# Kernel optimization log

Hardware: AMD Instinct MI355X
Metric: run time of the kernel (lower is better)

Reference implementation:

```python
import jax, jax.numpy as jnp
import numpy as np

N, H_DIM, LATENT, MLP_H, F_OUT = 256, 128, 128, 256, 16
SUPP = 0.5  # ancestor_suppression_strength
EPS = 1e-12


def setup_inputs() -> dict:
    key = jax.random.key(0)
    ks = jax.random.split(key, 12)
    def w(k, shape):
        fan_in = shape[0]
        return jax.random.normal(k, shape, jnp.float32) / np.sqrt(fan_in)
    return {
        'z': jax.random.normal(ks[0], (LATENT,), jnp.float32),
        'targets': jax.random.randint(ks[1], (N, N), 0, 2, jnp.int32),
        'pos_emb': jax.random.normal(ks[2], (N, H_DIM), jnp.float32),
        'Ws1': w(ks[3], (H_DIM, H_DIM)),
        'Wn1': w(ks[4], (H_DIM, H_DIM)),
        'b1': jnp.zeros((H_DIM,), jnp.float32),
        'Ws2': w(ks[5], (H_DIM, H_DIM)),
        'Wn2': w(ks[6], (H_DIM, H_DIM)),
        'b2': jnp.zeros((H_DIM,), jnp.float32),
        'Wm1': w(ks[7], (LATENT + 3 * H_DIM, MLP_H)),
        'bm1': jnp.zeros((MLP_H,), jnp.float32),
        'Wm2': w(ks[8], (MLP_H, 1)),
        'bm2': jnp.zeros((1,), jnp.float32),
        'Wf': w(ks[9], (H_DIM, F_OUT)),
        'bf': jnp.zeros((F_OUT,), jnp.float32),
    }


def reference(z, targets, pos_emb, Ws1, Wn1, b1, Ws2, Wn2, b2,
              Wm1, bm1, Wm2, bm2, Wf, bf):
    tgt = jnp.tril(targets.astype(jnp.float32), -1)  # [N,N] strict lower: row=child, col=parent
    idx = jnp.arange(N)
    h0 = z  # decoder_init=None => hidden state init is z itself
    layers = ((Ws1, Wn1, b1), (Ws2, Wn2, b2))

    def gnn(Hs, M, active):
        # M[dst, src]: messages aggregated over incoming (parent) edges
        for Ws, Wn, b in layers:
            Hs = jax.nn.relu(Hs @ Ws + (M @ Hs) @ Wn + b) * active[:, None]
        return Hs

    def step(carry, t):
        Hs, anc, lp = carry
        Hs = Hs.at[t].set(h0 + pos_emb[t])          # new node t
        active = (idx <= t).astype(jnp.float32)
        M = tgt * (idx < t)[:, None].astype(jnp.float32)  # edges added in steps < t
        Hs = gnn(Hs, M, active)
        h_t = Hs[t]
        cand = (idx < t).astype(jnp.float32)        # candidate parents i < t
        mlp_in = jnp.concatenate([
            jnp.broadcast_to(h_t, (N, H_DIM)), Hs,
            jnp.broadcast_to(z, (N, LATENT)),
            jnp.broadcast_to(pos_emb[t], (N, H_DIM))], axis=1)
        logits = (jax.nn.relu(mlp_in @ Wm1 + bm1) @ Wm2 + bm2)[:, 0]
        probs = jax.nn.sigmoid(logits)
        # suppression[i] = prod_{j<t} (1 - s * anc[j][i])
        supp = jnp.prod(jnp.where((idx < t)[:, None], 1.0 - SUPP * anc, 1.0), axis=0)
        adj = probs * supp
        gt = tgt[t]
        logp = gt * jnp.log(adj + EPS) + (1.0 - gt) * jnp.log(1.0 - adj + EPS)
        lp = lp + jnp.sum(logp * cand)
        # ancestors of t = union over parents p of (anc[p] | {p})
        anc_t = jnp.minimum(1.0, gt @ anc + gt)
        anc = anc.at[t].set(anc_t)
        return (Hs, anc, lp), None

    H0 = jnp.zeros((N, H_DIM), jnp.float32).at[0].set(h0)
    anc0 = jnp.zeros((N, N), jnp.float32)
    (Hs, anc, lp), _ = jax.lax.scan(step, (H0, anc0, jnp.float32(0.0)), jnp.arange(1, N))
    # node_feature_decoder path: one more GNN pass over the full graph
    Hs = gnn(Hs, tgt, jnp.ones((N,), jnp.float32))
    X_out = Hs @ Wf + bf
    return tgt, X_out, lp
```

## Files before the change

kernel.cpp:

```cpp
#include <hip/hip_runtime.h>

#define NN 256
#define HD 128
#define GNN_NB 128
#define MLP_NB 64
#define NBLK 192
#define NTHR 512
#define D_HS 3
#define D_H1 2

#define HS_OFF 0
#define H1R_OFF 98304
#define PROG_OFF 163840
#define MF_OFF   (163840 + 4096)

#define STH_L 0
#define STM_L 256
#define PT_L  512
#define TGT_L 0
#define PTM_L 2048
#define PT3_L 10240
#define HC_L  11264
#define CT_L  11776
#define CZ_L  12032
#define W2_L  12288
#define HP_L  12544
#define PART_L 12800
#define ANC_L 13312
#define LP_L  13344
#define LDS_FLOATS 13360

__device__ __forceinline__ float2 ldc_f2(const float* p) {
    unsigned long long u = __hip_atomic_load((const unsigned long long*)p,
                                             __ATOMIC_RELAXED, __HIP_MEMORY_SCOPE_AGENT);
    float2 r;
    r.x = __uint_as_float((unsigned)u);
    r.y = __uint_as_float((unsigned)(u >> 32));
    return r;
}
__device__ __forceinline__ void stc_f(float* p, float v) {
    __hip_atomic_store((unsigned*)p, __float_as_uint(v),
                       __ATOMIC_RELAXED, __HIP_MEMORY_SCOPE_AGENT);
}
__device__ __forceinline__ unsigned ldf(const unsigned* p) {
    return __hip_atomic_load(p, __ATOMIC_RELAXED, __HIP_MEMORY_SCOPE_AGENT);
}
__device__ __forceinline__ void stf(unsigned* p, unsigned v) {
    __hip_atomic_store(p, v, __ATOMIC_RELAXED, __HIP_MEMORY_SCOPE_AGENT);
}

__device__ __forceinline__ void bar_lds() {
    asm volatile("s_waitcnt lgkmcnt(0)\n\ts_barrier" ::: "memory");
}

__device__ __forceinline__ void wait_gnn(const unsigned* prog, const unsigned* mf,
                                         int b, unsigned dataTh, unsigned ringTh, int mlpTh)
{
    const int tid = threadIdx.x;
    if (tid < GNN_NB) {
        const unsigned th = (tid < b) ? dataTh : ringTh;
        if (th)
            while (ldf(prog + tid * 32) < th) __builtin_amdgcn_s_sleep(1);
    } else if (tid < GNN_NB + MLP_NB) {
        if (mlpTh > 0)
            while ((int)ldf(mf + (tid - GNN_NB) * 32) < mlpTh) __builtin_amdgcn_s_sleep(1);
    }
    __syncthreads();
    asm volatile("" ::: "memory");
}

#define ISS(i) \
    float2 va##i, vb##i, vc##i, vd##i; \
    if ((i) < nst) { \
        const float* p_ = gsrc + (i) * 32 * HD; \
        if ((un >> (4 * (i)    )) & 1u) va##i = ldc_f2(p_); \
        if ((un >> (4 * (i) + 1)) & 1u) vb##i = ldc_f2(p_ + HD); \
        if ((un >> (4 * (i) + 2)) & 1u) vc##i = ldc_f2(p_ + 2 * HD); \
        if ((un >> (4 * (i) + 3)) & 1u) vd##i = ldc_f2(p_ + 3 * HD); \
    }
#define ACCP(v, b) { \
    const float f0_ = (float)((s0 >> (b)) & 1u); \
    const float f1_ = (float)((s1 >> (b)) & 1u); \
    m0.x = fmaf(f0_, v.x, m0.x); m0.y = fmaf(f0_, v.y, m0.y); \
    m1.x = fmaf(f1_, v.x, m1.x); m1.y = fmaf(f1_, v.y, m1.y); }
#define ACC1(v, b) if ((un >> (b)) & 1u) { ACCP(v, b) }
#define CNS(i) if ((i) < nst) { ACC1(va##i, 4*(i)) ACC1(vb##i, 4*(i)+1) \
                                ACC1(vc##i, 4*(i)+2) ACC1(vd##i, 4*(i)+3) }

__device__ __forceinline__ void layer(const float* src, float* dst, float bc,
    const float* z, const float* pos_emb, float* lds,
    const float (&wsA)[32], const float (&wnA)[32],
    unsigned mk0, unsigned mk1,
    int R0, int rmax, int tgate, int tnew, int lane, int wv, int tid, int c, int kbase)
{
    const int rmaxblk = min(rmax, R0 + 1);
    const int nst = (rmaxblk + 31) >> 5;
    const unsigned s0 = (R0     < tgate) ? mk0 : 0u;
    const unsigned s1 = (R0 + 1 < tgate) ? mk1 : 0u;
    const unsigned un = s0 | s1;

    if (tnew >= R0 && tnew < R0 + 2) {
        const int dr = tnew - R0;
        if (tid < HD) lds[STH_L + dr * HD + tid] = z[tid] + pos_emb[tnew * HD + tid];
    }

    const float* gsrc = src + wv * 4 * HD + 2 * lane;
    float2 m0 = make_float2(0.f, 0.f), m1 = m0;
    ISS(0) ISS(1) ISS(2) ISS(3) ISS(4) ISS(5) ISS(6) ISS(7)
    CNS(0) CNS(1) CNS(2) CNS(3) CNS(4) CNS(5) CNS(6) CNS(7)

    float* pt = lds + PT_L + (wv * 2) * HD + 2 * lane;
    *(float2*)pt = m0;
    *(float2*)(pt + HD) = m1;
    bar_lds();
    if (tid < 256) {
        const int dr = tid >> 7, k = tid & 127;
        float s = 0.f;
#pragma unroll
        for (int w = 0; w < 8; ++w) s += lds[PT_L + (w * 2 + dr) * HD + k];
        lds[STM_L + dr * HD + k] = s;
    }
    bar_lds();
    float acc0 = 0.f, acc1 = 0.f;
#pragma unroll
    for (int q = 0; q < 8; ++q) {
        const float4 h0 = *(const float4*)(lds + STH_L + kbase + 4 * q);
        const float4 mm0 = *(const float4*)(lds + STM_L + kbase + 4 * q);
        const float4 h1 = *(const float4*)(lds + STH_L + HD + kbase + 4 * q);
        const float4 mm1 = *(const float4*)(lds + STM_L + HD + kbase + 4 * q);
        acc0 = fmaf(h0.x, wsA[4*q],   fmaf(mm0.x, wnA[4*q],   acc0));
        acc0 = fmaf(h0.y, wsA[4*q+1], fmaf(mm0.y, wnA[4*q+1], acc0));
        acc0 = fmaf(h0.z, wsA[4*q+2], fmaf(mm0.z, wnA[4*q+2], acc0));
        acc0 = fmaf(h0.w, wsA[4*q+3], fmaf(mm0.w, wnA[4*q+3], acc0));
        acc1 = fmaf(h1.x, wsA[4*q],   fmaf(mm1.x, wnA[4*q],   acc1));
        acc1 = fmaf(h1.y, wsA[4*q+1], fmaf(mm1.y, wnA[4*q+1], acc1));
        acc1 = fmaf(h1.z, wsA[4*q+2], fmaf(mm1.z, wnA[4*q+2], acc1));
        acc1 = fmaf(h1.w, wsA[4*q+3], fmaf(mm1.w, wnA[4*q+3], acc1));
    }
    acc0 += __shfl_xor(acc0, 16); acc0 += __shfl_xor(acc0, 32);
    acc1 += __shfl_xor(acc1, 16); acc1 += __shfl_xor(acc1, 32);
    const float o0 = fmaxf(acc0 + bc, 0.f);
    const float o1 = fmaxf(acc1 + bc, 0.f);
    const int kg = lane >> 4;
    if (kg == 0) { if (R0     <= rmaxblk) stc_f(dst + R0 * HD + c, o0); }
    else if (kg == 1) { if (R0 + 1 <= rmaxblk) stc_f(dst + (R0 + 1) * HD + c, o1); }
    else if (kg == 2) lds[STH_L + c] = o0;
    else              lds[STH_L + HD + c] = o1;
}

__device__ __forceinline__ void ct_calc(const float* hsP, const float* pos_emb,
                                        const float* Wm1, float* lds, int s)
{
    const int tid = threadIdx.x;
    if (tid < 64) {
        const float2 v = ldc_f2(hsP + s * HD + 2 * tid);
        lds[HP_L + 2 * tid] = v.x; lds[HP_L + 2 * tid + 1] = v.y;
    } else if (tid < 128) {
        const int l2 = tid - 64;
        lds[HP_L + 128 + 2 * l2]     = pos_emb[s * HD + 2 * l2];
        lds[HP_L + 128 + 2 * l2 + 1] = pos_emb[s * HD + 2 * l2 + 1];
    }
    __syncthreads();
    const int c = tid & 255, half = tid >> 8;
    float acc = 0.f;
    const float* w = half ? (Wm1 + 384 * 256 + c) : (Wm1 + c);
    const float* hh = lds + HP_L + half * 128;
#pragma unroll 4
    for (int k = 0; k < HD; ++k) acc = fmaf(hh[k], w[k * 256], acc);
    lds[PART_L + half * 256 + c] = acc;
    __syncthreads();
    if (tid < 256)
        lds[CT_L + tid] = lds[CZ_L + tid] + lds[PART_L + tid] + lds[PART_L + 256 + tid];
}

__device__ __forceinline__ void mlp_step(const float* hsP, const float* bm2,
                                         const float4 (&wm)[16], float* lds, int mb, int s)
{
    const int tid = threadIdx.x, lane = tid & 63, wv = tid >> 6;
    const int ks = wv * 16;
    if (wv < 4) {
        const int i = 4 * mb + wv;
        float2 v = make_float2(0.f, 0.f);
        if (i < s) v = ldc_f2(hsP + i * HD + 2 * lane);
        *(float2*)(lds + HC_L + wv * HD + 2 * lane) = v;
    }
    __syncthreads();
    float4 a0 = make_float4(0.f, 0.f, 0.f, 0.f), a1 = a0, a2 = a0, a3 = a0;
#pragma unroll
    for (int kk = 0; kk < 16; ++kk) {
        const int k = ks + kk;
        const float h0 = lds[HC_L + 0 * HD + k];
        const float h1 = lds[HC_L + 1 * HD + k];
        const float h2 = lds[HC_L + 2 * HD + k];
        const float h3 = lds[HC_L + 3 * HD + k];
        const float4 w = wm[kk];
        a0.x = fmaf(h0, w.x, a0.x); a0.y = fmaf(h0, w.y, a0.y);
        a0.z = fmaf(h0, w.z, a0.z); a0.w = fmaf(h0, w.w, a0.w);
        a1.x = fmaf(h1, w.x, a1.x); a1.y = fmaf(h1, w.y, a1.y);
        a1.z = fmaf(h1, w.z, a1.z); a1.w = fmaf(h1, w.w, a1.w);
        a2.x = fmaf(h2, w.x, a2.x); a2.y = fmaf(h2, w.y, a2.y);
        a2.z = fmaf(h2, w.z, a2.z); a2.w = fmaf(h2, w.w, a2.w);
        a3.x = fmaf(h3, w.x, a3.x); a3.y = fmaf(h3, w.y, a3.y);
        a3.z = fmaf(h3, w.z, a3.z); a3.w = fmaf(h3, w.w, a3.w);
    }
    *(float4*)(lds + PTM_L + (wv * 4 + 0) * 256 + 4 * lane) = a0;
    *(float4*)(lds + PTM_L + (wv * 4 + 1) * 256 + 4 * lane) = a1;
    *(float4*)(lds + PTM_L + (wv * 4 + 2) * 256 + 4 * lane) = a2;
    *(float4*)(lds + PTM_L + (wv * 4 + 3) * 256 + 4 * lane) = a3;
    __syncthreads();
    {
        const int c = tid & 255, ci2 = (tid >> 8) * 2;
#pragma unroll
        for (int q = 0; q < 2; ++q) {
            const int ci = ci2 + q;
            float v = lds[CT_L + c];
#pragma unroll
            for (int w = 0; w < 8; ++w) v += lds[PTM_L + (w * 4 + ci) * 256 + c];
            lds[PT3_L + ci * 256 + c] = fmaxf(v, 0.f) * lds[W2_L + c];
        }
    }
    __syncthreads();
    if (wv < 4) {
        const int ci = wv, i = 4 * mb + ci;
        if (i < s) {
            float sd = lds[PT3_L + ci * 256 + lane] + lds[PT3_L + ci * 256 + 64 + lane]
                     + lds[PT3_L + ci * 256 + 128 + lane] + lds[PT3_L + ci * 256 + 192 + lane];
#pragma unroll
            for (int off = 32; off > 0; off >>= 1) sd += __shfl_xor(sd, off);
            if (lane == 0) {
                const unsigned* gtl = (const unsigned*)(lds + TGT_L) + s * 8;
                unsigned* ancl = (unsigned*)(lds + ANC_L);
                const float logit = sd + bm2[0];
                const float prob = 1.f / (1.f + expf(-logit));
                unsigned cnt = 0, has = 0;
#pragma unroll
                for (int w = 0; w < 8; ++w) {
                    const unsigned av = ancl[ci * 8 + w];
                    cnt += __popc(av);
                    has |= av & gtl[w];
                }
                const float supp = ldexpf(1.f, -(int)cnt);
                const float adj = prob * supp;
                const unsigned gt = (gtl[i >> 5] >> (i & 31)) & 1u;
                const float lpv = gt ? logf(adj + 1e-12f) : logf(1.f - adj + 1e-12f);
                atomicAdd((float*)(lds + LP_L), lpv);
                if (has | gt) ancl[ci * 8 + (s >> 5)] |= (1u << (s & 31));
            }
        }
    }
}

extern "C" __global__ void __launch_bounds__(NTHR)
fused_gnn(const float* z, const int* targets, const float* pos_emb,
          const float* Ws1, const float* Wn1, const float* b1,
          const float* Ws2, const float* Wn2, const float* b2,
          const float* Wm1, const float* bm1, const float* Wm2, const float* bm2,
          const float* Wf, const float* bf, float* out, float* ws)
{
    __shared__ __align__(16) float lds[LDS_FLOATS];
    const int b = blockIdx.x;
    const int tid = threadIdx.x, lane = tid & 63, wv = tid >> 6;

    unsigned* prog = (unsigned*)(ws + PROG_OFF);
    unsigned* mf   = (unsigned*)(ws + MF_OFF);
    float* lp_out = out + NN * NN + NN * 16;

    if (b < GNN_NB) {
        const int R0 = b * 2;
        const int c = 16 * wv + (lane & 15);
        const int kbase = 32 * (lane >> 4);
        float ws1[32], wn1[32], ws2[32], wn2[32];
#pragma unroll
        for (int i = 0; i < 32; ++i) {
            ws1[i] = Ws1[(kbase + i) * HD + c];
            wn1[i] = Wn1[(kbase + i) * HD + c];
            ws2[i] = Ws2[(kbase + i) * HD + c];
            wn2[i] = Wn2[(kbase + i) * HD + c];
        }
        const float b1c = b1[c], b2c = b2[c];
        unsigned mk0, mk1;
        {
            const int srcl = (lane < 32) ? (((lane >> 2) << 5) + wv * 4 + (lane & 3)) : 0;
#define BALLOT_MK(dr, dst) { \
            const int r_ = R0 + (dr); \
            const bool p_ = (lane < 32) && (srcl < r_) && (targets[r_ * NN + srcl] != 0); \
            const unsigned long long bm_ = __ballot(p_); \
            dst = (unsigned)__builtin_amdgcn_readfirstlane((int)(unsigned)bm_); }
            BALLOT_MK(0, mk0) BALLOT_MK(1, mk1)
#undef BALLOT_MK
        }
        if (tid < 256) lds[STH_L + tid] = (b == 0 && tid < HD) ? z[tid] : 0.f;
        if (tid < 256) {
            const int dr = tid >> 7, cc = tid & 127, r = R0 + dr;
            stc_f(ws + HS_OFF + r * HD + cc, (r == 0) ? z[cc] : 0.f);
        }
        if (wv < 2) {
            const int r = R0 + wv;
            const int4 tv = ((const int4*)(targets + r * NN))[lane];
            float4 ov;
            ov.x = (4 * lane     < r) ? (float)tv.x : 0.f;
            ov.y = (4 * lane + 1 < r) ? (float)tv.y : 0.f;
            ov.z = (4 * lane + 2 < r) ? (float)tv.z : 0.f;
            ov.w = (4 * lane + 3 < r) ? (float)tv.w : 0.f;
            ((float4*)(out + r * NN))[lane] = ov;
        }
        __syncthreads();
        if (tid == 0) stf(prog + b * 32, 1u);

        for (int t = 1; t <= 256; ++t) {
            const float* hsP = ws + HS_OFF + ((t - 1) % D_HS) * 32768;
            float* h1c = ws + H1R_OFF + (t & 1) * 32768;
            float* hsN = ws + HS_OFF + (t % D_HS) * 32768;
            const int rmax  = (t <= 255) ? t : 255;
            const int tgate = (t <= 255) ? t : 300;
            const int tnew  = (t <= 255) ? t : -1;
            const bool act = (R0 <= rmax);

            if (act) {
                wait_gnn(prog, mf, b, 2u * t - 1u,
                         (t > D_H1) ? (2u * (t - D_H1) + 1u) : 0u, 0);
                layer(hsP, h1c, b1c, z, pos_emb, lds, ws1, wn1,
                      mk0, mk1, R0, rmax, tgate, tnew, lane, wv, tid, c, kbase);
            }
            __syncthreads();
            if (tid == 0) stf(prog + b * 32, 2u * t);

            if (act) {
                wait_gnn(prog, mf, b, 2u * t,
                         (t > D_HS) ? (2u * (t - D_HS + 1)) : 0u, t - D_HS);
                layer(h1c, hsN, b2c, z, pos_emb, lds, ws2, wn2,
                      mk0, mk1, R0, rmax, tgate, -1, lane, wv, tid, c, kbase);
            }
            __syncthreads();
            if (tid == 0) stf(prog + b * 32, 2u * t + 1u);
        }

        if (wv < 2) {
            const int r = R0 + wv;
            const float* strow = lds + STH_L + wv * HD;
            const int f = lane & 15, kp = lane >> 4;
            float sacc = 0.f;
#pragma unroll
            for (int k = 0; k < 32; ++k)
                sacc = fmaf(strow[kp * 32 + k], Wf[(kp * 32 + k) * 16 + f], sacc);
            sacc += __shfl_xor(sacc, 16);
            sacc += __shfl_xor(sacc, 32);
            if (lane < 16) out[NN * NN + r * 16 + f] = sacc + bf[f];
        }
    } else {
        const int mb = b - GNN_NB;
        const int ks = wv * 16;
        float4 wm[16];
#pragma unroll
        for (int kk = 0; kk < 16; ++kk)
            wm[kk] = *(const float4*)(Wm1 + (128 + ks + kk) * 256 + 4 * lane);
        {
            unsigned* tg = (unsigned*)(lds + TGT_L);
            for (int rr = 0; rr < 32; ++rr) {
                const int r = wv * 32 + rr;
#pragma unroll
                for (int q = 0; q < 4; ++q) {
                    const int j = q * 64 + lane;
                    const unsigned long long bm = __ballot(j < r && targets[r * NN + j] != 0);
                    if (lane == 0) {
                        tg[r * 8 + 2 * q]     = (unsigned)bm;
                        tg[r * 8 + 2 * q + 1] = (unsigned)(bm >> 32);
                    }
                }
            }
        }
        if (tid < 256) {
            lds[W2_L + tid] = Wm2[tid];
            float acc = bm1[tid];
            for (int k = 0; k < HD; ++k) acc = fmaf(z[k], Wm1[(256 + k) * 256 + tid], acc);
            lds[CZ_L + tid] = acc;
        }
        if (tid < 32) ((unsigned*)(lds + ANC_L))[tid] = 0u;
        if (tid == 0) lds[LP_L] = 0.f;

        for (int s = 1; s <= 255; ++s) {
            if (tid < GNN_NB) {
                const unsigned need = 2u * (unsigned)s + 1u;
                while (ldf(prog + tid * 32) < need) __builtin_amdgcn_s_sleep(1);
            }
            __syncthreads();
            const float* hsP = ws + HS_OFF + (s % D_HS) * 32768;
            if (4 * mb < s) {
                ct_calc(hsP, pos_emb, Wm1, lds, s);
                __syncthreads();
                mlp_step(hsP, bm2, wm, lds, mb, s);
            }
            __syncthreads();
            if (tid == 0) stf(mf + mb * 32, (unsigned)s);
        }
        __syncthreads();
        if (tid == 0) atomicAdd(lp_out, lds[LP_L]);
    }
}

extern "C" void kernel_launch(void* const* d_in, const int* in_sizes, int n_in,
                              void* d_out, int out_size, void* d_ws, size_t ws_size,
                              hipStream_t stream)
{
    const float* z       = (const float*)d_in[0];
    const int*   targets = (const int*)d_in[1];
    const float* pos_emb = (const float*)d_in[2];
    const float* Ws1     = (const float*)d_in[3];
    const float* Wn1     = (const float*)d_in[4];
    const float* b1      = (const float*)d_in[5];
    const float* Ws2     = (const float*)d_in[6];
    const float* Wn2     = (const float*)d_in[7];
    const float* b2      = (const float*)d_in[8];
    const float* Wm1     = (const float*)d_in[9];
    const float* bm1     = (const float*)d_in[10];
    const float* Wm2     = (const float*)d_in[11];
    const float* bm2     = (const float*)d_in[12];
    const float* Wf      = (const float*)d_in[13];
    const float* bf      = (const float*)d_in[14];
    float* out = (float*)d_out;
    float* ws  = (float*)d_ws;

    (void)hipMemsetAsync(ws + PROG_OFF, 0, (GNN_NB + MLP_NB) * 32 * sizeof(unsigned), stream);
    (void)hipMemsetAsync(out + NN * NN + NN * 16, 0, sizeof(float), stream);

    void* args[17] = {
        (void*)&z, (void*)&targets, (void*)&pos_emb,
        (void*)&Ws1, (void*)&Wn1, (void*)&b1,
        (void*)&Ws2, (void*)&Wn2, (void*)&b2,
        (void*)&Wm1, (void*)&bm1, (void*)&Wm2, (void*)&bm2,
        (void*)&Wf, (void*)&bf, (void*)&out, (void*)&ws
    };
    (void)hipLaunchCooperativeKernel((const void*)fused_gnn, dim3(NBLK), dim3(NTHR),
                                     args, 0, stream);
}
```

Baseline: 1.869 ms.

## Switch to per-wave progress flags and cached polling with double-buffered LDS state

Result: slower. 2.275 ms (+21.8%).

```diff
diff --git a/kernel.cpp b/kernel.cpp
--- a/kernel.cpp
+++ b/kernel.cpp
@@ -6,17 +6,15 @@
 #define MLP_NB 64
 #define NBLK 192
 #define NTHR 512
-#define D_HS 3
-#define D_H1 2
 
 #define HS_OFF 0
 #define H1R_OFF 98304
-#define PROG_OFF 163840
-#define MF_OFF   (163840 + 4096)
+#define PROG8_OFF 163840
+#define MF_OFF (163840 + 32768)
 
 #define STH_L 0
-#define STM_L 256
-#define PT_L  512
+#define STM_L 512
+#define PT_L  768
 #define TGT_L 0
 #define PTM_L 2048
 #define PT3_L 10240
@@ -53,21 +51,12 @@
     asm volatile("s_waitcnt lgkmcnt(0)\n\ts_barrier" ::: "memory");
 }
 
-__device__ __forceinline__ void wait_gnn(const unsigned* prog, const unsigned* mf,
-                                         int b, unsigned dataTh, unsigned ringTh, int mlpTh)
-{
-    const int tid = threadIdx.x;
-    if (tid < GNN_NB) {
-        const unsigned th = (tid < b) ? dataTh : ringTh;
-        if (th)
-            while (ldf(prog + tid * 32) < th) __builtin_amdgcn_s_sleep(1);
-    } else if (tid < GNN_NB + MLP_NB) {
-        if (mlpTh > 0)
-            while ((int)ldf(mf + (tid - GNN_NB) * 32) < mlpTh) __builtin_amdgcn_s_sleep(1);
-    }
-    __syncthreads();
-    asm volatile("" ::: "memory");
-}
+#define POLLW(ptr, th, cache) \
+    if ((cache) < (th)) { \
+        unsigned v_; \
+        for (;;) { v_ = ldf(ptr); if (v_ >= (th)) break; __builtin_amdgcn_s_sleep(1); } \
+        (cache) = v_; \
+    }
 
 #define ISS(i) \
     float2 va##i, vb##i, vc##i, vd##i; \
@@ -91,17 +80,20 @@
     const float* z, const float* pos_emb, float* lds,
     const float (&wsA)[32], const float (&wnA)[32],
     unsigned mk0, unsigned mk1,
-    int R0, int rmax, int tgate, int tnew, int lane, int wv, int tid, int c, int kbase)
+    int R0, int rmax, int tgate, int tnew, int lane, int wv, int tid, int c, int kbase,
+    int pr)
 {
     const int rmaxblk = min(rmax, R0 + 1);
     const int nst = (rmaxblk + 31) >> 5;
     const unsigned s0 = (R0     < tgate) ? mk0 : 0u;
     const unsigned s1 = (R0 + 1 < tgate) ? mk1 : 0u;
     const unsigned un = s0 | s1;
+    float* sthR = lds + STH_L + pr * 256;
+    float* sthW = lds + STH_L + (pr ^ 1) * 256;
 
     if (tnew >= R0 && tnew < R0 + 2) {
         const int dr = tnew - R0;
-        if (tid < HD) lds[STH_L + dr * HD + tid] = z[tid] + pos_emb[tnew * HD + tid];
+        if (tid < HD) sthR[dr * HD + tid] = z[tid] + pos_emb[tnew * HD + tid];
     }
 
     const float* gsrc = src + wv * 4 * HD + 2 * lane;
@@ -124,9 +116,9 @@
     float acc0 = 0.f, acc1 = 0.f;
 #pragma unroll
     for (int q = 0; q < 8; ++q) {
-        const float4 h0 = *(const float4*)(lds + STH_L + kbase + 4 * q);
+        const float4 h0 = *(const float4*)(sthR + kbase + 4 * q);
         const float4 mm0 = *(const float4*)(lds + STM_L + kbase + 4 * q);
-        const float4 h1 = *(const float4*)(lds + STH_L + HD + kbase + 4 * q);
+        const float4 h1 = *(const float4*)(sthR + HD + kbase + 4 * q);
         const float4 mm1 = *(const float4*)(lds + STM_L + HD + kbase + 4 * q);
         acc0 = fmaf(h0.x, wsA[4*q],   fmaf(mm0.x, wnA[4*q],   acc0));
         acc0 = fmaf(h0.y, wsA[4*q+1], fmaf(mm0.y, wnA[4*q+1], acc0));
@@ -144,8 +136,8 @@
     const int kg = lane >> 4;
     if (kg == 0) { if (R0     <= rmaxblk) stc_f(dst + R0 * HD + c, o0); }
     else if (kg == 1) { if (R0 + 1 <= rmaxblk) stc_f(dst + (R0 + 1) * HD + c, o1); }
-    else if (kg == 2) lds[STH_L + c] = o0;
-    else              lds[STH_L + HD + c] = o1;
+    else if (kg == 2) sthW[c] = o0;
+    else              sthW[HD + c] = o1;
 }
 
 __device__ __forceinline__ void ct_calc(const float* hsP, const float* pos_emb,
@@ -261,8 +253,8 @@
     const int b = blockIdx.x;
     const int tid = threadIdx.x, lane = tid & 63, wv = tid >> 6;
 
-    unsigned* prog = (unsigned*)(ws + PROG_OFF);
-    unsigned* mf   = (unsigned*)(ws + MF_OFF);
+    unsigned* prog8 = (unsigned*)(ws + PROG8_OFF);
+    unsigned* mf    = (unsigned*)(ws + MF_OFF);
     float* lp_out = out + NN * NN + NN * 16;
 
     if (b < GNN_NB) {
@@ -304,35 +296,73 @@
             ov.w = (4 * lane + 3 < r) ? (float)tv.w : 0.f;
             ((float4*)(out + r * NN))[lane] = ov;
         }
+        asm volatile("s_waitcnt vmcnt(0)" ::: "memory");
+        if (lane == 0) stf(prog8 + (b * 8 + wv) * 32, 1u);
+
+        const int bA = tid >> 3, bB = 64 + (tid >> 3);
+        unsigned sA = 0, sB = 0;
+        int      sM = 0;
+
+        {
+            if (bA < b) POLLW(prog8 + tid * 32, 1u, sA)
+            if (bB < b) POLLW(prog8 + (tid + 512) * 32, 1u, sB)
+        }
+        asm volatile("" ::: "memory");
         __syncthreads();
-        if (tid == 0) stf(prog + b * 32, 1u);
 
         for (int t = 1; t <= 256; ++t) {
-            const float* hsP = ws + HS_OFF + ((t - 1) % D_HS) * 32768;
+            const float* hsP = ws + HS_OFF + ((t - 1) % 3) * 32768;
             float* h1c = ws + H1R_OFF + (t & 1) * 32768;
-            float* hsN = ws + HS_OFF + (t % D_HS) * 32768;
+            float* hsN = ws + HS_OFF + (t % 3) * 32768;
             const int rmax  = (t <= 255) ? t : 255;
             const int tgate = (t <= 255) ? t : 300;
             const int tnew  = (t <= 255) ? t : -1;
             const bool act = (R0 <= rmax);
 
+            if (act)
+                layer(hsP, h1c, b1c, z, pos_emb, lds, ws1, wn1, mk0, mk1,
+                      R0, rmax, tgate, tnew, lane, wv, tid, c, kbase, 0);
+            asm volatile("s_waitcnt vmcnt(0)" ::: "memory");
+            if (lane == 0) stf(prog8 + (b * 8 + wv) * 32, 2u * t);
             if (act) {
-                wait_gnn(prog, mf, b, 2u * t - 1u,
-                         (t > D_H1) ? (2u * (t - D_H1) + 1u) : 0u, 0);
-                layer(hsP, h1c, b1c, z, pos_emb, lds, ws1, wn1,
-                      mk0, mk1, R0, rmax, tgate, tnew, lane, wv, tid, c, kbase);
-            }
+                const unsigned dataTh = 2u * t;
+                const unsigned ringTh = (t > 3) ? (2u * (t - 2)) : 0u;
+                const unsigned thA = (bA < b) ? dataTh : ringTh;
+                const unsigned thB = (bB < b) ? dataTh : ringTh;
+                if (thA) POLLW(prog8 + tid * 32, thA, sA)
+                if (thB) POLLW(prog8 + (tid + 512) * 32, thB, sB)
+                const int mlpTh = t - 3;
+                const bool ownRow = (mlpTh > 0) && ((mlpTh >> 1) == b);
+                if (tid < 64 && mlpTh > 0 && (tid == (b >> 1) || ownRow)) {
+                    if (sM < mlpTh) {
+                        int v;
+                        for (;;) {
+                            v = (int)ldf(mf + tid * 32);
+                            if (v >= mlpTh) break;
+                            __builtin_amdgcn_s_sleep(1);
+                        }
+                        sM = v;
+                    }
+                }
+            }
+            asm volatile("" ::: "memory");
             __syncthreads();
-            if (tid == 0) stf(prog + b * 32, 2u * t);
-
-            if (act) {
-                wait_gnn(prog, mf, b, 2u * t,
-                         (t > D_HS) ? (2u * (t - D_HS + 1)) : 0u, t - D_HS);
-                layer(h1c, hsN, b2c, z, pos_emb, lds, ws2, wn2,
-                      mk0, mk1, R0, rmax, tgate, -1, lane, wv, tid, c, kbase);
-            }
+
+            if (act)
+                layer(h1c, hsN, b2c, z, pos_emb, lds, ws2, wn2, mk0, mk1,
+                      R0, rmax, tgate, -1, lane, wv, tid, c, kbase, 1);
+            asm volatile("s_waitcnt vmcnt(0)" ::: "memory");
+            if (lane == 0) stf(prog8 + (b * 8 + wv) * 32, 2u * t + 1u);
+            if (t < 256 && R0 <= t + 1) {
+                const unsigned dataTh = 2u * t + 1u;
+                const unsigned ringTh = (t >= 2) ? (2u * (t - 1) + 1u) : 0u;
+                const unsigned thA = (bA < b) ? dataTh : ringTh;
+                const unsigned thB = (bB < b) ? dataTh : ringTh;
+                if (thA) POLLW(prog8 + tid * 32, thA, sA)
+                if (thB) POLLW(prog8 + (tid + 512) * 32, thB, sB)
+            }
+            asm volatile("" ::: "memory");
             __syncthreads();
-            if (tid == 0) stf(prog + b * 32, 2u * t + 1u);
         }
 
         if (wv < 2) {
@@ -377,14 +407,25 @@
         }
         if (tid < 32) ((unsigned*)(lds + ANC_L))[tid] = 0u;
         if (tid == 0) lds[LP_L] = 0.f;
-
+        __syncthreads();
+
+        unsigned cA = 0, cB = 0;
         for (int s = 1; s <= 255; ++s) {
-            if (tid < GNN_NB) {
+            if (4 * mb < s && tid < 24) {
                 const unsigned need = 2u * (unsigned)s + 1u;
-                while (ldf(prog + tid * 32) < need) __builtin_amdgcn_s_sleep(1);
+                const int which = tid >> 3, wvf = tid & 7;
+                if (which == 0) {
+                    POLLW(prog8 + ((2 * mb) * 8 + wvf) * 32, need, cA)
+                } else if (which == 1) {
+                    POLLW(prog8 + ((2 * mb + 1) * 8 + wvf) * 32, need, cB)
+                } else {
+                    const unsigned* p = prog8 + ((s >> 1) * 8 + wvf) * 32;
+                    unsigned v;
+                    for (;;) { v = ldf(p); if (v >= need) break; __builtin_amdgcn_s_sleep(1); }
+                }
             }
             __syncthreads();
-            const float* hsP = ws + HS_OFF + (s % D_HS) * 32768;
+            const float* hsP = ws + HS_OFF + (s % 3) * 32768;
             if (4 * mb < s) {
                 ct_calc(hsP, pos_emb, Wm1, lds, s);
                 __syncthreads();
@@ -420,7 +461,7 @@
     float* out = (float*)d_out;
     float* ws  = (float*)d_ws;
 
-    (void)hipMemsetAsync(ws + PROG_OFF, 0, (GNN_NB + MLP_NB) * 32 * sizeof(unsigned), stream);
+    (void)hipMemsetAsync(ws + PROG8_OFF, 0, (128 * 8 + 64) * 32 * sizeof(unsigned), stream);
     (void)hipMemsetAsync(out + NN * NN + NN * 16, 0, sizeof(float), stream);
 
     void* args[17] = {
```
